# Optimization experiments

Measured on AMD Instinct MI355X. Metric: run time of the kernel, lower is better.

## Reference

```python
import jax, jax.numpy as jnp
import numpy as np

TOP_K = 2  # k experts per token


def setup_inputs() -> dict:
    key = jax.random.key(0)
    ks = jax.random.split(key, 6)
    B, L, D, E, F = 2, 2048, 1024, 8, 4096
    x = jax.random.normal(ks[0], (B, L, D), dtype=jnp.float32)
    Wg = jax.random.normal(ks[1], (D, E), dtype=jnp.float32) * (D ** -0.5)
    W1 = jax.random.normal(ks[2], (E, D, F), dtype=jnp.float32) * (D ** -0.5)
    b1 = jnp.zeros((E, F), dtype=jnp.float32)
    W2 = jax.random.normal(ks[3], (E, F, D), dtype=jnp.float32) * (F ** -0.5)
    b2 = jnp.zeros((E, D), dtype=jnp.float32)
    return {"x": x, "Wg": Wg, "W1": W1, "b1": b1, "W2": W2, "b2": b2}


def reference(x, Wg, W1, b1, W2, b2):
    b, l, d = x.shape
    E = Wg.shape[1]
    xt = x.reshape(b * l, d)                      # (N, D)
    N = xt.shape[0]
    # Router: sigmoid gate, top-k (gate weights are NOT renormalized in the source)
    S = jax.nn.sigmoid(xt @ Wg)                   # (N, E)
    G, I = jax.lax.top_k(S, TOP_K)                # (N, k) each
    # Dense equivalent of per-expert gather-MLP-scatter: run every expert
    # on every token, then combine with the sparse top-k routing weights.
    h = jax.nn.gelu(jnp.einsum('nd,edf->enf', xt, W1) + b1[:, None, :])  # (E, N, F)
    y = jnp.einsum('enf,efd->end', h, W2) + b2[:, None, :]               # (E, N, D)
    # combine[n, e] = sum of gate values for slots routed to expert e
    combine = jnp.zeros((N, E), dtype=x.dtype).at[jnp.arange(N)[:, None], I].add(G)
    out = jnp.einsum('ne,end->nd', combine, y)    # (N, D)
    return out.reshape(b, l, d)
```

## Files before the change

### kernel.cpp

```cpp
#include <hip/hip_runtime.h>
#include <math.h>

typedef __bf16 bf16_t;
typedef __attribute__((ext_vector_type(8))) __bf16 bf16x8;
typedef __attribute__((ext_vector_type(4))) __bf16 bf16x4;
typedef __attribute__((ext_vector_type(4))) float f32x4;

#define NTOK 4096
#define DDIM 1024
#define FDIM 4096
#define NEXP 8
#define CAP  4096
#define HROWS (2*NTOK + 128)

#define GLOAD_LDS16(g, l) \
  __builtin_amdgcn_global_load_lds((__attribute__((address_space(1))) void*)(g), \
                                   (__attribute__((address_space(3))) void*)(l), 16, 0, 0)

__global__ __launch_bounds__(256) void zero_kernel(float4* __restrict__ out4, int n4,
                                                   int* __restrict__ cnts) {
  int i = blockIdx.x * 256 + threadIdx.x;
  if (i < n4) out4[i] = make_float4(0.f, 0.f, 0.f, 0.f);
  if (i < NEXP) cnts[i] = 0;
}

__global__ __launch_bounds__(256) void cvt_x_kernel(const float4* __restrict__ in,
                                                    bf16x4* __restrict__ outp, int n4) {
  int i = blockIdx.x * 256 + threadIdx.x;
  if (i < n4) {
    float4 v = in[i];
    bf16x4 o;
    o.x = (bf16_t)v.x; o.y = (bf16_t)v.y; o.z = (bf16_t)v.z; o.w = (bf16_t)v.w;
    outp[i] = o;
  }
}

__global__ __launch_bounds__(256) void transpose_cvt(const float* __restrict__ in,
                                                     bf16_t* __restrict__ outp,
                                                     int R, int C) {
  __shared__ float tile[32][33];
  int e = blockIdx.z;
  const float* ip = in + (size_t)e * R * C;
  bf16_t* op = outp + (size_t)e * R * C;
  int c0 = blockIdx.x * 32, r0 = blockIdx.y * 32;
  int tx = threadIdx.x & 31, ty = threadIdx.x >> 5;
#pragma unroll
  for (int i = 0; i < 4; i++)
    tile[ty + i * 8][tx] = ip[(size_t)(r0 + ty + i * 8) * C + c0 + tx];
  __syncthreads();
#pragma unroll
  for (int i = 0; i < 4; i++)
    op[(size_t)(c0 + ty + i * 8) * R + r0 + tx] = (bf16_t)tile[tx][ty + i * 8];
}

__global__ __launch_bounds__(256) void router_kernel(const float* __restrict__ x,
                                                     const float* __restrict__ Wg,
                                                     int* __restrict__ tokL,
                                                     float* __restrict__ gateL,
                                                     int* __restrict__ cnts) {
  int wid = threadIdx.x >> 6, lane = threadIdx.x & 63;
  int n = blockIdx.x * 4 + wid;
  const float* xr = x + (size_t)n * DDIM;
  double acc[NEXP];
#pragma unroll
  for (int e = 0; e < NEXP; e++) acc[e] = 0.0;
  for (int i = 0; i < DDIM / 64; i++) {
    int d = i * 64 + lane;
    float xv = xr[d];
    const float* wr = Wg + (size_t)d * NEXP;
#pragma unroll
    for (int e = 0; e < NEXP; e++) acc[e] += (double)xv * (double)wr[e];
  }
#pragma unroll
  for (int e = 0; e < NEXP; e++) {
    double v = acc[e];
#pragma unroll
    for (int off = 32; off; off >>= 1) v += __shfl_xor(v, off);
    acc[e] = v;
  }
  if (lane == 0) {
    int i1 = -1, i2 = -1;
    double s1 = -1e300, s2 = -1e300;
#pragma unroll
    for (int e = 0; e < NEXP; e++) {
      double v = acc[e];
      if (v > s1) { s2 = s1; i2 = i1; s1 = v; i1 = e; }
      else if (v > s2) { s2 = v; i2 = e; }
    }
    float g1 = 1.0f / (1.0f + expf((float)(-s1)));
    float g2 = 1.0f / (1.0f + expf((float)(-s2)));
    int p1 = atomicAdd(&cnts[i1], 1);
    tokL[i1 * CAP + p1] = n; gateL[i1 * CAP + p1] = g1;
    int p2 = atomicAdd(&cnts[i2], 1);
    tokL[i2 * CAP + p2] = n; gateL[i2 * CAP + p2] = g2;
  }
}

__global__ void offs_kernel(const int* __restrict__ cnts, int* __restrict__ offs) {
  if (threadIdx.x == 0) {
    int s = 0;
    for (int e = 0; e < NEXP; e++) { offs[e] = s; s += cnts[e]; }
    offs[NEXP] = s;
  }
}

__global__ __launch_bounds__(256) void gemm1_kernel(
    const bf16_t* __restrict__ xbf, const bf16_t* __restrict__ wt1,
    const float* __restrict__ b1, const int* __restrict__ tokL,
    const int* __restrict__ cnts, const int* __restrict__ offs,
    bf16_t* __restrict__ H) {
  const int e = blockIdx.z;
  const int cnt = cnts[e];
  const int m0 = blockIdx.y * 128;
  if (m0 >= cnt) return;
  const int n0 = blockIdx.x * 128;
  const int t = threadIdx.x;

  __shared__ alignas(16) bf16_t As[128 * 32];
  __shared__ alignas(16) bf16_t Bs[128 * 32];

  const int sr = t >> 2;
  const int sc = (t & 3) * 8;
  const int r0 = m0 + sr, r1 = m0 + sr + 64;
  const int tok0 = (r0 < cnt) ? tokL[e * CAP + r0] : 0;
  const int tok1 = (r1 < cnt) ? tokL[e * CAP + r1] : 0;
  const bf16_t* gA0 = xbf + (size_t)tok0 * DDIM + sc;
  const bf16_t* gA1 = xbf + (size_t)tok1 * DDIM + sc;
  const bf16_t* wte = wt1 + (size_t)e * FDIM * DDIM;
  const bf16_t* gB0 = wte + (size_t)(n0 + sr) * DDIM + sc;
  const bf16_t* gB1 = wte + (size_t)(n0 + sr + 64) * DDIM + sc;
  bf16_t* lA0 = As + t * 8; bf16_t* lA1 = As + 2048 + t * 8;
  bf16_t* lB0 = Bs + t * 8; bf16_t* lB1 = Bs + 2048 + t * 8;

  const int lane = t & 63, w = t >> 6;
  const int wm = (w >> 1) * 64, wn = (w & 1) * 64;
  const int lid = lane & 15, quad = lane >> 4;

  f32x4 acc[4][4] = {};
  for (int kk = 0; kk < DDIM; kk += 32) {
    GLOAD_LDS16(gA0 + kk, lA0);
    GLOAD_LDS16(gA1 + kk, lA1);
    GLOAD_LDS16(gB0 + kk, lB0);
    GLOAD_LDS16(gB1 + kk, lB1);
    __syncthreads();
    bf16x8 af[4], bfm[4];
#pragma unroll
    for (int i = 0; i < 4; i++)
      af[i] = *(const bf16x8*)(As + (wm + i * 16 + lid) * 32 + quad * 8);
#pragma unroll
    for (int j = 0; j < 4; j++)
      bfm[j] = *(const bf16x8*)(Bs + (wn + j * 16 + lid) * 32 + quad * 8);
#pragma unroll
    for (int i = 0; i < 4; i++)
#pragma unroll
      for (int j = 0; j < 4; j++)
        acc[i][j] = __builtin_amdgcn_mfma_f32_16x16x32_bf16(af[i], bfm[j], acc[i][j], 0, 0, 0);
    __syncthreads();
  }

  const float* b1e = b1 + (size_t)e * FDIM;
  const int offe = offs[e];
#pragma unroll
  for (int i = 0; i < 4; i++) {
#pragma unroll
    for (int reg = 0; reg < 4; reg++) {
      int pos = m0 + wm + i * 16 + quad * 4 + reg;
      if (pos >= cnt) continue;
      size_t hrow = (size_t)(offe + pos);
#pragma unroll
      for (int j = 0; j < 4; j++) {
        int col = n0 + wn + j * 16 + lid;
        float v = acc[i][j][reg] + b1e[col];
        float u = 0.7978845608028654f * (v + 0.044715f * v * v * v);
        float g = 0.5f * v * (1.0f + tanhf(u));
        H[hrow * FDIM + col] = (bf16_t)g;
      }
    }
  }
}

__global__ __launch_bounds__(256) void gemm2_kernel(
    const bf16_t* __restrict__ H, const bf16_t* __restrict__ wt2,
    const float* __restrict__ b2, const int* __restrict__ tokL,
    const float* __restrict__ gateL, const int* __restrict__ cnts,
    const int* __restrict__ offs, float* __restrict__ out) {
  const int e = blockIdx.z;
  const int cnt = cnts[e];
  const int m0 = blockIdx.y * 128;
  if (m0 >= cnt) return;
  const int n0 = blockIdx.x * 128;
  const int t = threadIdx.x;
  const int offe = offs[e];

  __shared__ alignas(16) bf16_t As[128 * 32];
  __shared__ alignas(16) bf16_t Bs[128 * 32];

  const int sr = t >> 2;
  const int sc = (t & 3) * 8;
  const bf16_t* gA0 = H + (size_t)(offe + m0 + sr) * FDIM + sc;
  const bf16_t* gA1 = H + (size_t)(offe + m0 + sr + 64) * FDIM + sc;
  const bf16_t* wte = wt2 + (size_t)e * DDIM * FDIM;
  const bf16_t* gB0 = wte + (size_t)(n0 + sr) * FDIM + sc;
  const bf16_t* gB1 = wte + (size_t)(n0 + sr + 64) * FDIM + sc;
  bf16_t* lA0 = As + t * 8; bf16_t* lA1 = As + 2048 + t * 8;
  bf16_t* lB0 = Bs + t * 8; bf16_t* lB1 = Bs + 2048 + t * 8;

  const int lane = t & 63, w = t >> 6;
  const int wm = (w >> 1) * 64, wn = (w & 1) * 64;
  const int lid = lane & 15, quad = lane >> 4;

  f32x4 acc[4][4] = {};
  for (int kk = 0; kk < FDIM; kk += 32) {
    GLOAD_LDS16(gA0 + kk, lA0);
    GLOAD_LDS16(gA1 + kk, lA1);
    GLOAD_LDS16(gB0 + kk, lB0);
    GLOAD_LDS16(gB1 + kk, lB1);
    __syncthreads();
    bf16x8 af[4], bfm[4];
#pragma unroll
    for (int i = 0; i < 4; i++)
      af[i] = *(const bf16x8*)(As + (wm + i * 16 + lid) * 32 + quad * 8);
#pragma unroll
    for (int j = 0; j < 4; j++)
      bfm[j] = *(const bf16x8*)(Bs + (wn + j * 16 + lid) * 32 + quad * 8);
#pragma unroll
    for (int i = 0; i < 4; i++)
#pragma unroll
      for (int j = 0; j < 4; j++)
        acc[i][j] = __builtin_amdgcn_mfma_f32_16x16x32_bf16(af[i], bfm[j], acc[i][j], 0, 0, 0);
    __syncthreads();
  }

  const float* b2e = b2 + (size_t)e * DDIM;
#pragma unroll
  for (int i = 0; i < 4; i++) {
#pragma unroll
    for (int reg = 0; reg < 4; reg++) {
      int pos = m0 + wm + i * 16 + quad * 4 + reg;
      if (pos >= cnt) continue;
      int tok = tokL[e * CAP + pos];
      float gate = gateL[e * CAP + pos];
#pragma unroll
      for (int j = 0; j < 4; j++) {
        int col = n0 + wn + j * 16 + lid;
        float v = acc[i][j][reg] + b2e[col];
        atomicAdd(out + (size_t)tok * DDIM + col, gate * v);
      }
    }
  }
}

extern "C" void kernel_launch(void* const* d_in, const int* in_sizes, int n_in,
                              void* d_out, int out_size, void* d_ws, size_t ws_size,
                              hipStream_t stream) {
  const float* x  = (const float*)d_in[0];
  const float* Wg = (const float*)d_in[1];
  const float* W1 = (const float*)d_in[2];
  const float* b1 = (const float*)d_in[3];
  const float* W2 = (const float*)d_in[4];
  const float* b2 = (const float*)d_in[5];
  float* out = (float*)d_out;

  char* ws = (char*)d_ws;
  size_t off = 0;
  auto alloc = [&](size_t bytes) -> void* {
    void* p = (void*)(ws + off);
    off += (bytes + 255) & ~(size_t)255;
    return p;
  };
  bf16_t* xbf   = (bf16_t*)alloc((size_t)NTOK * DDIM * 2);
  bf16_t* wt1   = (bf16_t*)alloc((size_t)NEXP * FDIM * DDIM * 2);
  bf16_t* wt2   = (bf16_t*)alloc((size_t)NEXP * DDIM * FDIM * 2);
  bf16_t* H     = (bf16_t*)alloc((size_t)HROWS * FDIM * 2);
  int*    tokL  = (int*)alloc((size_t)NEXP * CAP * 4);
  float*  gateL = (float*)alloc((size_t)NEXP * CAP * 4);
  int*    cnts  = (int*)alloc(64);
  int*    offs  = (int*)alloc(64);
  if (off > ws_size) return;

  const int n4 = NTOK * DDIM / 4;
  zero_kernel<<<(n4 + 255) / 256, 256, 0, stream>>>((float4*)out, n4, cnts);
  cvt_x_kernel<<<(n4 + 255) / 256, 256, 0, stream>>>((const float4*)x, (bf16x4*)xbf, n4);
  transpose_cvt<<<dim3(FDIM / 32, DDIM / 32, NEXP), 256, 0, stream>>>(W1, wt1, DDIM, FDIM);
  transpose_cvt<<<dim3(DDIM / 32, FDIM / 32, NEXP), 256, 0, stream>>>(W2, wt2, FDIM, DDIM);
  router_kernel<<<NTOK / 4, 256, 0, stream>>>(x, Wg, tokL, gateL, cnts);
  offs_kernel<<<1, 64, 0, stream>>>(cnts, offs);
  gemm1_kernel<<<dim3(FDIM / 128, CAP / 128, NEXP), 256, 0, stream>>>(
      xbf, wt1, b1, tokL, cnts, offs, H);
  gemm2_kernel<<<dim3(DDIM / 128, CAP / 128, NEXP), 256, 0, stream>>>(
      H, wt2, b2, tokL, gateL, cnts, offs, out);
}
```

Before: 728.4 us.

## Split-K gemm2, fuse init kernels, widen transpose tiles, fast GELU

```diff
diff --git a/kernel.cpp b/kernel.cpp
--- a/kernel.cpp
+++ b/kernel.cpp
@@ -12,45 +12,64 @@
 #define NEXP 8
 #define CAP  4096
 #define HROWS (2*NTOK + 128)
+#define SPLITK2 4
 
 #define GLOAD_LDS16(g, l) \
   __builtin_amdgcn_global_load_lds((__attribute__((address_space(1))) void*)(g), \
                                    (__attribute__((address_space(3))) void*)(l), 16, 0, 0)
 
-__global__ __launch_bounds__(256) void zero_kernel(float4* __restrict__ out4, int n4,
-                                                   int* __restrict__ cnts) {
-  int i = blockIdx.x * 256 + threadIdx.x;
-  if (i < n4) out4[i] = make_float4(0.f, 0.f, 0.f, 0.f);
-  if (i < NEXP) cnts[i] = 0;
-}
-
-__global__ __launch_bounds__(256) void cvt_x_kernel(const float4* __restrict__ in,
-                                                    bf16x4* __restrict__ outp, int n4) {
+__device__ __forceinline__ float fast_gelu(float v) {
+  float u = 0.7978845608028654f * (v + 0.044715f * v * v * v);
+  float uc = fminf(fmaxf(u, -10.f), 10.f);
+  float t = __builtin_amdgcn_exp2f(2.885390081777927f * uc);
+  float th = (t - 1.f) * __builtin_amdgcn_rcpf(t + 1.f);
+  return 0.5f * v * (1.0f + th);
+}
+
+__global__ __launch_bounds__(256) void init_kernel(const float4* __restrict__ x4,
+                                                   float4* __restrict__ out4,
+                                                   bf16x4* __restrict__ xbf4,
+                                                   int n4, int* __restrict__ cnts) {
   int i = blockIdx.x * 256 + threadIdx.x;
   if (i < n4) {
-    float4 v = in[i];
+    out4[i] = make_float4(0.f, 0.f, 0.f, 0.f);
+    float4 v = x4[i];
     bf16x4 o;
     o.x = (bf16_t)v.x; o.y = (bf16_t)v.y; o.z = (bf16_t)v.z; o.w = (bf16_t)v.w;
-    outp[i] = o;
-  }
+    xbf4[i] = o;
+  }
+  if (i < NEXP) cnts[i] = 0;
 }
 
 __global__ __launch_bounds__(256) void transpose_cvt(const float* __restrict__ in,
                                                      bf16_t* __restrict__ outp,
                                                      int R, int C) {
-  __shared__ float tile[32][33];
+  __shared__ float tile[64][65];
   int e = blockIdx.z;
   const float* ip = in + (size_t)e * R * C;
   bf16_t* op = outp + (size_t)e * R * C;
-  int c0 = blockIdx.x * 32, r0 = blockIdx.y * 32;
-  int tx = threadIdx.x & 31, ty = threadIdx.x >> 5;
-#pragma unroll
-  for (int i = 0; i < 4; i++)
-    tile[ty + i * 8][tx] = ip[(size_t)(r0 + ty + i * 8) * C + c0 + tx];
+  int c0 = blockIdx.x * 64, r0 = blockIdx.y * 64;
+  int rr = threadIdx.x >> 4;
+  int cc = (threadIdx.x & 15) * 4;
+#pragma unroll
+  for (int p = 0; p < 4; p++) {
+    float4 v = *(const float4*)(ip + (size_t)(r0 + p * 16 + rr) * C + c0 + cc);
+    tile[p * 16 + rr][cc + 0] = v.x;
+    tile[p * 16 + rr][cc + 1] = v.y;
+    tile[p * 16 + rr][cc + 2] = v.z;
+    tile[p * 16 + rr][cc + 3] = v.w;
+  }
   __syncthreads();
-#pragma unroll
-  for (int i = 0; i < 4; i++)
-    op[(size_t)(c0 + ty + i * 8) * R + r0 + tx] = (bf16_t)tile[tx][ty + i * 8];
+  int c = threadIdx.x >> 3;
+  int r8 = (threadIdx.x & 7) * 8;
+#pragma unroll
+  for (int p = 0; p < 2; p++) {
+    int cp = c + p * 32;
+    bf16x8 o;
+#pragma unroll
+    for (int i = 0; i < 8; i++) o[i] = (bf16_t)tile[r8 + i][cp];
+    *(bf16x8*)(op + (size_t)(c0 + cp) * R + r0 + r8) = o;
+  }
 }
 
 __global__ __launch_bounds__(256) void router_kernel(const float* __restrict__ x,
@@ -171,9 +190,7 @@
       for (int j = 0; j < 4; j++) {
         int col = n0 + wn + j * 16 + lid;
         float v = acc[i][j][reg] + b1e[col];
-        float u = 0.7978845608028654f * (v + 0.044715f * v * v * v);
-        float g = 0.5f * v * (1.0f + tanhf(u));
-        H[hrow * FDIM + col] = (bf16_t)g;
+        H[hrow * FDIM + col] = (bf16_t)fast_gelu(v);
       }
     }
   }
@@ -186,22 +203,25 @@
     const int* __restrict__ offs, float* __restrict__ out) {
   const int e = blockIdx.z;
   const int cnt = cnts[e];
-  const int m0 = blockIdx.y * 128;
+  const int by = blockIdx.y;
+  const int m0 = (by / SPLITK2) * 128;
+  const int split = by % SPLITK2;
   if (m0 >= cnt) return;
   const int n0 = blockIdx.x * 128;
   const int t = threadIdx.x;
   const int offe = offs[e];
+  const int k0 = split * (FDIM / SPLITK2);
 
   __shared__ alignas(16) bf16_t As[128 * 32];
   __shared__ alignas(16) bf16_t Bs[128 * 32];
 
   const int sr = t >> 2;
   const int sc = (t & 3) * 8;
-  const bf16_t* gA0 = H + (size_t)(offe + m0 + sr) * FDIM + sc;
-  const bf16_t* gA1 = H + (size_t)(offe + m0 + sr + 64) * FDIM + sc;
+  const bf16_t* gA0 = H + (size_t)(offe + m0 + sr) * FDIM + sc + k0;
+  const bf16_t* gA1 = H + (size_t)(offe + m0 + sr + 64) * FDIM + sc + k0;
   const bf16_t* wte = wt2 + (size_t)e * DDIM * FDIM;
-  const bf16_t* gB0 = wte + (size_t)(n0 + sr) * FDIM + sc;
-  const bf16_t* gB1 = wte + (size_t)(n0 + sr + 64) * FDIM + sc;
+  const bf16_t* gB0 = wte + (size_t)(n0 + sr) * FDIM + sc + k0;
+  const bf16_t* gB1 = wte + (size_t)(n0 + sr + 64) * FDIM + sc + k0;
   bf16_t* lA0 = As + t * 8; bf16_t* lA1 = As + 2048 + t * 8;
   bf16_t* lB0 = Bs + t * 8; bf16_t* lB1 = Bs + 2048 + t * 8;
 
@@ -210,7 +230,7 @@
   const int lid = lane & 15, quad = lane >> 4;
 
   f32x4 acc[4][4] = {};
-  for (int kk = 0; kk < FDIM; kk += 32) {
+  for (int kk = 0; kk < FDIM / SPLITK2; kk += 32) {
     GLOAD_LDS16(gA0 + kk, lA0);
     GLOAD_LDS16(gA1 + kk, lA1);
     GLOAD_LDS16(gB0 + kk, lB0);
@@ -243,7 +263,7 @@
 #pragma unroll
       for (int j = 0; j < 4; j++) {
         int col = n0 + wn + j * 16 + lid;
-        float v = acc[i][j][reg] + b2e[col];
+        float v = acc[i][j][reg] + ((split == 0) ? b2e[col] : 0.f);
         atomicAdd(out + (size_t)tok * DDIM + col, gate * v);
       }
     }
@@ -279,14 +299,14 @@
   if (off > ws_size) return;
 
   const int n4 = NTOK * DDIM / 4;
-  zero_kernel<<<(n4 + 255) / 256, 256, 0, stream>>>((float4*)out, n4, cnts);
-  cvt_x_kernel<<<(n4 + 255) / 256, 256, 0, stream>>>((const float4*)x, (bf16x4*)xbf, n4);
-  transpose_cvt<<<dim3(FDIM / 32, DDIM / 32, NEXP), 256, 0, stream>>>(W1, wt1, DDIM, FDIM);
-  transpose_cvt<<<dim3(DDIM / 32, FDIM / 32, NEXP), 256, 0, stream>>>(W2, wt2, FDIM, DDIM);
+  init_kernel<<<(n4 + 255) / 256, 256, 0, stream>>>((const float4*)x, (float4*)out,
+                                                    (bf16x4*)xbf, n4, cnts);
+  transpose_cvt<<<dim3(FDIM / 64, DDIM / 64, NEXP), 256, 0, stream>>>(W1, wt1, DDIM, FDIM);
+  transpose_cvt<<<dim3(DDIM / 64, FDIM / 64, NEXP), 256, 0, stream>>>(W2, wt2, FDIM, DDIM);
   router_kernel<<<NTOK / 4, 256, 0, stream>>>(x, Wg, tokL, gateL, cnts);
   offs_kernel<<<1, 64, 0, stream>>>(cnts, offs);
   gemm1_kernel<<<dim3(FDIM / 128, CAP / 128, NEXP), 256, 0, stream>>>(
       xbf, wt1, b1, tokL, cnts, offs, H);
-  gemm2_kernel<<<dim3(DDIM / 128, CAP / 128, NEXP), 256, 0, stream>>>(
+  gemm2_kernel<<<dim3(DDIM / 128, (CAP / 128) * SPLITK2, NEXP), 256, 0, stream>>>(
       H, wt2, b2, tokL, gateL, cnts, offs, out);
 }
```

Result: slower. 746.1 us (+2.4%).
